# Performance work log

Measured on AMD Instinct MI355X. Metric: run time of the kernel, lower is better.

## Reference

```python
import jax, jax.numpy as jnp
import numpy as np
from jax import lax

NUM_SUPERNODES = 1024
KNN_K = 16
MIN_GRIPPER = 16
MIN_MASK = 8
GRIP_START = 0
GRIP_RADIUS = 0.1
NEG_INF = -jnp.inf


def _take(a, idx):
    return jnp.take_along_axis(a, idx, axis=1)


def _scatter_or(idx, keep, Bf, N):
    # OR `keep` into a fresh [Bf,N] bool mask at positions idx (mirrors torch scatter_)
    b = jnp.arange(Bf)[:, None]
    return jnp.zeros((Bf, N), dtype=bool).at[b, idx].max(keep)


def _cdist(a, b):
    # a [B,M,3], b [B,N,3] -> [B,M,N] euclidean
    d2 = (jnp.sum(a * a, -1)[:, :, None] + jnp.sum(b * b, -1)[:, None, :]
          - 2.0 * jnp.einsum('bmd,bnd->bmn', a, b))
    return jnp.sqrt(jnp.maximum(d2, 0.0))


def _sample_supernodes(xyz, valid, state, mask_id, extra_scores, global_scores):
    Bf, N, _ = xyz.shape
    M = NUM_SUPERNODES
    valid = valid.astype(bool)
    row_has_valid = valid.any(axis=1)
    first_valid = jnp.argmax(valid, axis=1).astype(jnp.int32)  # [Bf]

    # ---- gripper quota: nearest points to gripper xyz (within radius if any) ----
    k_grip = min(MIN_GRIPPER, M)
    gxyz = state[:, GRIP_START:GRIP_START + 3]
    gdist = jnp.linalg.norm(xyz - gxyz[:, None, :], axis=-1)  # [Bf,N]
    in_radius = gdist <= GRIP_RADIUS
    has_radius = (valid & in_radius).any(axis=1, keepdims=True)
    eligible = valid & (in_radius | ~has_radius)
    dist_rank = jnp.where(eligible, gdist, jnp.inf)
    neg_vals, grip_idx = lax.top_k(-dist_rank, k_grip)
    grip_vals = -neg_vals
    grip_keep = jnp.isfinite(grip_vals) & row_has_valid[:, None]
    head_idx = jnp.where(grip_keep, grip_idx, first_valid[:, None])
    head_bucket = jnp.where(grip_keep, 1, -1)
    selected = _scatter_or(grip_idx, grip_keep, Bf, N)

    remaining = M - k_grip
    # ---- mask-instance quota: one point per mask id (dedup via sort) ----
    mask_cand = valid & ~selected
    sentinel = jnp.iinfo(mask_id.dtype).max
    mask_key = jnp.where(mask_cand, mask_id, sentinel)
    sort_idx = jnp.argsort(mask_key, axis=1)
    sorted_valid = _take(mask_cand, sort_idx)
    sorted_mask = _take(mask_id, sort_idx)
    first_for_id = jnp.concatenate(
        [sorted_valid[:, :1],
         sorted_valid[:, 1:] & (sorted_mask[:, 1:] != sorted_mask[:, :-1])], axis=1)
    pos = jnp.arange(N, dtype=jnp.float32)[None, :]
    mask_scores = jnp.where(first_for_id, -pos, NEG_INF)
    mask_vals, mask_pos = lax.top_k(mask_scores, remaining)
    mask_idx = _take(sort_idx, mask_pos)
    mask_keep = jnp.isfinite(mask_vals) & row_has_valid[:, None]
    selected_after_mask = selected | _scatter_or(mask_idx, mask_keep, Bf, N)

    # ---- extra random mask supernodes to guarantee min_mask quota ----
    k_extra = min(MIN_MASK, remaining)
    es = jnp.where(valid & ~selected_after_mask, extra_scores, NEG_INF)
    extra_vals, extra_idx = lax.top_k(es, k_extra)
    extra_keep = jnp.isfinite(extra_vals) & row_has_valid[:, None]
    use_extra = ~mask_keep[:, :k_extra] & extra_keep
    mask_idx = mask_idx.at[:, :k_extra].set(
        jnp.where(use_extra, extra_idx, mask_idx[:, :k_extra]))
    mask_keep = mask_keep.at[:, :k_extra].set(mask_keep[:, :k_extra] | use_extra)

    # ---- global random fill ----
    selected_for_global = selected | _scatter_or(mask_idx, mask_keep, Bf, N)
    gs = jnp.where(valid & ~selected_for_global, global_scores, NEG_INF)
    gvals, gidx = lax.top_k(gs, remaining)
    gkeep = jnp.isfinite(gvals) & row_has_valid[:, None]
    fill_idx = jnp.where(mask_keep, mask_idx,
                         jnp.where(gkeep, gidx, first_valid[:, None]))
    fill_bucket = jnp.where(mask_keep, 2, jnp.where(gkeep, 0, -1))

    out_idx = jnp.concatenate([head_idx, fill_idx], axis=1)
    out_bucket = jnp.concatenate([head_bucket, fill_bucket], axis=1)
    out_valid = _take(valid, out_idx) & row_has_valid[:, None]
    out_bucket = jnp.where(out_valid, out_bucket, -1)
    return out_idx, out_valid, out_bucket


def setup_inputs() -> dict:
    key = jax.random.key(0)
    ks = jax.random.split(key, 6)
    Bf, N, C = 8, 16384, 64
    return {
        'x': jax.random.normal(ks[0], (Bf, N, C), dtype=jnp.float32),
        'xyz': jax.random.normal(ks[1], (Bf, N, 3), dtype=jnp.float32),
        'valid': jnp.ones((Bf, N), dtype=bool),
        'state': jax.random.normal(ks[2], (Bf, 8), dtype=jnp.float32),
        'mask_id': jax.random.randint(ks[3], (Bf, N), 0, 32, dtype=jnp.int32),
        'extra_scores': jax.random.uniform(ks[4], (Bf, N), dtype=jnp.float32),
        'global_scores': jax.random.uniform(ks[5], (Bf, N), dtype=jnp.float32),
    }


def reference(x, xyz, valid, state, mask_id, extra_scores, global_scores):
    Bf, N, C = x.shape
    out_idx, out_valid, out_bucket = _sample_supernodes(
        xyz, valid, state, mask_id, extra_scores, global_scores)
    # gather_points
    supernode_xyz = _take(xyz, out_idx[:, :, None].repeat(3, axis=2))  # [Bf,M,3]
    # build_knn_neighbors: masked cdist + topk smallest
    dist = _cdist(supernode_xyz.astype(jnp.float32), xyz.astype(jnp.float32))
    dist = jnp.where(valid.astype(bool)[:, None, :], dist, jnp.inf)
    neg_vals, neighbor_idx = lax.top_k(-dist, KNN_K)
    neighbor_mask = jnp.isfinite(-neg_vals)  # [Bf,M,K]
    # gather_neighbors
    b = jnp.arange(Bf)[:, None, None]
    neighbor_feats = x[b, neighbor_idx]  # [Bf,M,K,C]
    return (neighbor_feats, supernode_xyz, neighbor_mask,
            out_idx, out_valid, out_bucket)
```

## Files before the change

kernel.cpp:

```cpp
#include <hip/hip_runtime.h>
#include <math.h>

typedef unsigned long long u64;
typedef unsigned int u32;

#define BF 8
#define NPTS 16384
#define M_SN 1024
#define CCH 64
#define KNN 16
#define NTHR1 1024
#define KPER 16
#define TBL 4096
#define CCAP 2048
#define REM 1008

constexpr size_t O0 = 0;
constexpr size_t O1 = 8388608;
constexpr size_t O2 = 8413184;
constexpr size_t O3 = 8544256;
constexpr size_t O4 = 8552448;
constexpr size_t O5 = 8560640;

#define PW_OFF ((size_t)256)
#define PW_BYTES ((size_t)BF * NPTS * 16)
#define SEG1_BYTES ((size_t)BF * M_SN * KNN * 8)

__device__ __forceinline__ bool is_valid_el(const void* vp, int mode, long long i) {
  if (mode == 1) return ((const unsigned char*)vp)[i] != 0;
  if (mode == 2) return ((const float*)vp)[i] != 0.0f;
  return ((const int*)vp)[i] != 0;
}

__device__ __forceinline__ u32 desc_enc(float f) {
  u32 u = __float_as_uint(f);
  u32 s = (u & 0x80000000u) ? ~u : (u | 0x80000000u);
  return ~s;
}
__device__ __forceinline__ bool enc_finite(u32 d) {
  u32 s = ~d;
  u32 u = (s & 0x80000000u) ? (s & 0x7FFFFFFFu) : ~s;
  return (u & 0x7F800000u) != 0x7F800000u;
}

__device__ __forceinline__ u64 wave_min_u64(u64 v) {
#pragma unroll
  for (int d = 32; d >= 1; d >>= 1) {
    u32 lo = __shfl_xor((u32)(v & 0xFFFFFFFFu), d, 64);
    u32 hi = __shfl_xor((u32)(v >> 32), d, 64);
    u64 o = ((u64)hi << 32) | lo;
    if (o < v) v = o;
  }
  return v;
}

__device__ __forceinline__ u64 block_min_u64(u64 v, u64* red16, int t) {
  v = wave_min_u64(v);
  if ((t & 63) == 0) red16[t >> 6] = v;
  __syncthreads();
  if (t < 64) {
    u64 x = red16[t & 15];
    x = wave_min_u64(x);
    if (t == 0) red16[0] = x;
  }
  __syncthreads();
  u64 r = red16[0];
  __syncthreads();
  return r;
}

__device__ __forceinline__ int block_excl_scan(int val, int* scanb, int t, int* tot) {
  int incl = val;
#pragma unroll
  for (int d = 1; d < 64; d <<= 1) {
    int v = __shfl_up(incl, d, 64);
    if ((t & 63) >= d) incl += v;
  }
  if ((t & 63) == 63) scanb[t >> 6] = incl;
  __syncthreads();
  if (t < 64) {
    int ws = (t < 16) ? scanb[t] : 0;
#pragma unroll
    for (int d = 1; d < 16; d <<= 1) {
      int v = __shfl_up(ws, d, 64);
      if ((t & 63) >= d) ws += v;
    }
    if (t < 16) scanb[16 + t] = ws;
  }
  __syncthreads();
  int wv = t >> 6;
  int base = (wv == 0) ? 0 : scanb[16 + wv - 1];
  *tot = scanb[16 + 15];
  int r = base + incl - val;
  __syncthreads();
  return r;
}

template<bool ASC, bool SHIFTBIN>
__device__ __forceinline__ void topk_select(const u32* ek, const u32* bk, u32 cmask,
    int Twant, int* table, u64* cand, int* scanb, int* sh, int* outArr, int t) {
  for (int j = t; j < TBL; j += NTHR1) table[j] = 0;
  if (t == 6) sh[6] = 0x7FFFFFFF;
  if (t == 7) sh[7] = 1;
  __syncthreads();
#pragma unroll
  for (int k = 0; k < KPER; k++) {
    if ((cmask >> k) & 1u) {
      int bin = SHIFTBIN ? (int)(ek[k] >> 20) : (int)bk[k];
      atomicAdd(&table[bin], 1);
    }
  }
  __syncthreads();
  int c_[4]; int c4 = 0;
#pragma unroll
  for (int q = 0; q < 4; q++) { c_[q] = table[4 * t + q]; c4 += c_[q]; }
  int htot;
  int cum = block_excl_scan(c4, scanb, t, &htot);
  const int T = min(Twant, htot);
  int e_ = cum;
#pragma unroll
  for (int q = 0; q < 4; q++) {
    int nx = e_ + c_[q];
    if (T > 0 && e_ < T && nx >= T) atomicMin(&sh[6], 4 * t + q);
    table[4 * t + q] = e_;
    e_ = nx;
  }
  __syncthreads();
  if (T <= 0) return;
  const int B = sh[6];
#pragma unroll
  for (int k = 0; k < KPER; k++) {
    if ((cmask >> k) & 1u) {
      int bin = SHIFTBIN ? (int)(ek[k] >> 20) : (int)bk[k];
      if (bin <= B) {
        int pos = atomicAdd(&table[bin], 1);
        if (pos < CCAP)
          cand[pos] = ((u64)ek[k] << 32) | ((u64)(u32)bin << 14) | (u32)(k * NTHR1 + t);
      }
    }
  }
  __syncthreads();
  const int nc = table[B];
  if (nc <= CCAP) {
    for (int c = t; c < nc; c += NTHR1) {
      u64 key = cand[c];
      int bin = (int)((key >> 14) & 0xFFFu);
      int s = bin ? table[bin - 1] : 0;
      int e2 = table[bin];
      int r = s;
      for (int j = s; j < e2; j++) r += (cand[j] < key);
      if (r < T) {
        u32 enc = (u32)(key >> 32);
        int ix = (int)(key & 0x3FFFu);
        bool fin = ASC ? (enc < 0x7F800000u) : enc_finite(enc);
        outArr[r] = fin ? ix : (ix | (int)0x80000000);
      }
    }
  } else {
    if (t == 0) sh[7] = 0;
  }
  __syncthreads();
}

__global__ void detect_valid(const unsigned* __restrict__ w, int nwords, int* __restrict__ flag) {
  __shared__ int cls;
  int t = threadIdx.x;
  if (t == 0) cls = 0;
  __syncthreads();
  int local = 0;
  for (int i = t; i < nwords; i += blockDim.x) {
    unsigned v = w[i];
    if (v == 0x3F800000u) local = 2;
    else if (v != 0u && v != 1u) local = max(local, 1);
  }
  if (local) atomicMax(&cls, local);
  __syncthreads();
  if (t == 0) flag[0] = cls;
}

__global__ __launch_bounds__(1024)
void sample_kernel(const float* __restrict__ xyz, const void* __restrict__ validp,
                   const float* __restrict__ state, const int* __restrict__ mask_id,
                   const float* __restrict__ extra, const float* __restrict__ glob,
                   int vwords, float4* __restrict__ pw, float* __restrict__ out) {
  __shared__ u64 red16[16];
  __shared__ int table[TBL];
  __shared__ int scanb[32];
  __shared__ int mpick[REM];
  __shared__ u64 cand[CCAP];
  __shared__ int gsorted[REM];
  __shared__ int head_i[16];
  __shared__ int head_bk[16];
  __shared__ int sh[8];

  const int b = blockIdx.x, t = threadIdx.x;
  const float* xyzb = xyz + (size_t)b * NPTS * 3;
  const int* midb = mask_id + (size_t)b * NPTS;
  const float* exb = extra + (size_t)b * NPTS;
  const float* glb = glob + (size_t)b * NPTS;

  if (t < 8) sh[t] = 0;
  if (t == 1) sh[1] = 0x7FFFFFFF;
  if (t < 16) gsorted[t] = -1;
  __syncthreads();

  {
    const unsigned* w = (const unsigned*)validp;
    int local = 0;
    for (int i = t; i < vwords; i += NTHR1) {
      unsigned vv = w[i];
      if (vv == 0x3F800000u) local = 2;
      else if (vv != 0u && vv != 1u) local = max(local, 1);
    }
    if (local) atomicMax(&sh[3], local);
  }
  __syncthreads();
  const int vmode = sh[3];

  u32 vbits = 0;
#pragma unroll
  for (int k = 0; k < KPER; k++) {
    int i = k * NTHR1 + t;
    if (is_valid_el(validp, vmode, (long long)b * NPTS + i)) vbits |= 1u << k;
  }
  if (vbits) {
    atomicOr(&sh[0], 1);
    atomicMin(&sh[1], (__ffs(vbits) - 1) * NTHR1 + t);
  }

  float gx = state[b * 8 + 0], gy = state[b * 8 + 1], gz = state[b * 8 + 2];
  float gd[KPER];
  u32 inr = 0;
#pragma unroll
  for (int k = 0; k < KPER; k++) {
    int i = k * NTHR1 + t;
    float px = xyzb[3 * i], py = xyzb[3 * i + 1], pz = xyzb[3 * i + 2];
    float dx = px - gx, dy = py - gy, dz = pz - gz;
    float d = sqrtf((dx * dx + dy * dy) + dz * dz);
    gd[k] = d;
    bool vb = (vbits >> k) & 1u;
    if (vb && d <= 0.1f) inr |= 1u << k;
    if (pw) {
      float sb = __fadd_rn(__fadd_rn(__fmul_rn(px, px), __fmul_rn(py, py)), __fmul_rn(pz, pz));
      pw[(size_t)b * NPTS + i] = make_float4(px, py, pz, vb ? sb : INFINITY);
    }
  }
  if (inr) atomicOr(&sh[2], 1);
  __syncthreads();

  const int rhv = sh[0];
  const int first_valid = rhv ? sh[1] : 0;
  const u32 elig = vbits & (sh[2] ? inr : 0xFFFFu);
  u32 sel = 0;

  {
    u32 ek[KPER];
#pragma unroll
    for (int k = 0; k < KPER; k++) ek[k] = __float_as_uint(gd[k]);
    topk_select<true, true>(ek, nullptr, elig, 16, table, cand, scanb, sh, gsorted, t);
    if (sh[7]) {
      if (t < 16) {
        int g = gsorted[t];
        head_i[t] = (g >= 0) ? g : first_valid;
        head_bk[t] = (g >= 0) ? 1 : -1;
      }
      __syncthreads();
      for (int j = 0; j < 16; j++) {
        if (head_bk[j] == 1) {
          int ix = head_i[j];
          if ((ix & (NTHR1 - 1)) == t) sel |= 1u << (ix >> 10);
        }
      }
    } else {
      for (int it = 0; it < 16; ++it) {
        u64 best = ~0ull;
#pragma unroll
        for (int k = 0; k < KPER; k++) {
          if (((elig >> k) & 1u) && !((sel >> k) & 1u)) {
            u64 key = ((u64)__float_as_uint(gd[k]) << 32) | (u32)(k * NTHR1 + t);
            if (key < best) best = key;
          }
        }
        u64 w = block_min_u64(best, red16, t);
        bool keep = (w >> 32) < 0x7F800000ull;
        int idx = (int)(w & 0xFFFFFFFFu);
        if (t == 0) { head_i[it] = keep ? idx : first_valid; head_bk[it] = keep ? 1 : -1; }
        if (keep && (idx & (NTHR1 - 1)) == t) sel |= 1u << (idx >> 10);
      }
      __syncthreads();
    }
  }

  for (int j = t; j < TBL; j += NTHR1) table[j] = 0x7FFFFFFF;
  __syncthreads();
#pragma unroll
  for (int k = 0; k < KPER; k++) {
    if (((vbits >> k) & 1u) && !((sel >> k) & 1u)) {
      int i = k * NTHR1 + t;
      int id = midb[i];
      if ((u32)id < TBL) atomicMin(&table[id], i);
    }
  }
  __syncthreads();
  int cnt = 0;
#pragma unroll
  for (int q = 0; q < 4; q++) cnt += (table[4 * t + q] != 0x7FFFFFFF);
  int mtot;
  int excl = block_excl_scan(cnt, scanb, t, &mtot);
  {
    int pos = excl;
#pragma unroll
    for (int q = 0; q < 4; q++) {
      int v = table[4 * t + q];
      if (v != 0x7FFFFFFF) { if (pos < REM) mpick[pos] = v; pos++; }
    }
  }
  __syncthreads();
  const int nm = min(mtot, REM);
  for (int j = 0; j < nm; j++) {
    int p = mpick[j];
    if ((p & (NTHR1 - 1)) == t) sel |= 1u << (p >> 10);
  }

  u32 extra_used = 0;
  if (nm < 8 && rhv) {
    u32 extrbits = 0;
    for (int j = 0; j < 8; j++) {
      u64 best = ~0ull;
#pragma unroll
      for (int k = 0; k < KPER; k++) {
        if (((vbits >> k) & 1u) && !((sel >> k) & 1u) && !((extrbits >> k) & 1u)) {
          int i = k * NTHR1 + t;
          u64 key = ((u64)desc_enc(exb[i]) << 32) | (u32)i;
          if (key < best) best = key;
        }
      }
      u64 w = block_min_u64(best, red16, t);
      if (w == ~0ull) break;
      int idx = (int)(w & 0xFFFFFFFFu);
      bool fin = enc_finite((u32)(w >> 32));
      if ((idx & (NTHR1 - 1)) == t) extrbits |= 1u << (idx >> 10);
      if (j >= nm && fin) {
        extra_used |= 1u << j;
        if (t == 0) mpick[j] = idx;
        if ((idx & (NTHR1 - 1)) == t) sel |= 1u << (idx >> 10);
      }
    }
    __syncthreads();
  }

  {
    u32 cbits = vbits & ~sel;
    u32 ek[KPER], bk[KPER];
#pragma unroll
    for (int k = 0; k < KPER; k++) {
      if ((cbits >> k) & 1u) {
        float f = glb[k * NTHR1 + t];
        ek[k] = desc_enc(f);
        float g = fminf(fmaxf(f, 0.0f), 0.99999994f);
        bk[k] = 4095u - (u32)(g * 4096.0f);
      } else { ek[k] = 0xFFFFFFFFu; bk[k] = 4095u; }
    }
    for (int j = t; j < REM; j += NTHR1) gsorted[j] = -1;
    topk_select<false, false>(ek, bk, cbits, REM, table, cand, scanb, sh, gsorted, t);
    if (!sh[7]) {
      u32 gext = 0;
      for (int j = 0; j < REM; j++) {
        u64 best = ~0ull;
#pragma unroll
        for (int k = 0; k < KPER; k++) {
          if (((cbits >> k) & 1u) && !((gext >> k) & 1u)) {
            u64 key = ((u64)ek[k] << 32) | (u32)(k * NTHR1 + t);
            if (key < best) best = key;
          }
        }
        u64 w = block_min_u64(best, red16, t);
        if (w == ~0ull) break;
        int idx = (int)(w & 0xFFFFFFFFu);
        if ((idx & (NTHR1 - 1)) == t) gext |= 1u << (idx >> 10);
        if (t == 0) gsorted[j] = enc_finite((u32)(w >> 32)) ? idx : (idx | (int)0x80000000);
      }
      __syncthreads();
    }
  }

  {
    int slot = t;
    int idx, bucket;
    if (slot < 16) {
      idx = head_i[slot];
      bucket = head_bk[slot];
    } else {
      int jj = slot - 16;
      bool mk = (jj < nm) || (jj < 8 && ((extra_used >> jj) & 1u));
      if (mk) { idx = mpick[jj]; bucket = 2; }
      else {
        int g = gsorted[jj];
        if (rhv && g >= 0) { idx = g; bucket = 0; }
        else { idx = first_valid; bucket = -1; }
      }
    }
    bool ov = rhv && is_valid_el(validp, vmode, (long long)b * NPTS + idx);
    int ob = ov ? bucket : -1;
    size_t o = (size_t)b * M_SN + slot;
    out[O3 + o] = (float)idx;
    out[O4 + o] = ov ? 1.0f : 0.0f;
    out[O5 + o] = (float)ob;
    out[O1 + 3 * o + 0] = xyzb[3 * idx + 0];
    out[O1 + 3 * o + 1] = xyzb[3 * idx + 1];
    out[O1 + 3 * o + 2] = xyzb[3 * idx + 2];
  }
}

#define NTHR2 256
#define CH 1024
#define SPG 2
#define SNBLK 16

__global__ __launch_bounds__(256)
void knn_kernel(const float* __restrict__ x, const float* __restrict__ xyz,
                const void* __restrict__ validp, const int* __restrict__ flagp,
                const float4* __restrict__ pw, u64* __restrict__ wnws, int nseg,
                float* __restrict__ out) {
  __shared__ __align__(16) float4 st[CH];
  __shared__ u64 wnl[SNBLK * KNN];

  const int b = blockIdx.x >> 6;
  const int snblk = blockIdx.x & 63;
  const int seg = blockIdx.y;
  const int t = threadIdx.x;
  const int g = t >> 5;
  const int sub = t & 31;
  const int lanebase = t & 32;
  const int m0 = snblk * SNBLK + g * SPG;
  const float* xyzb = xyz + (size_t)b * NPTS * 3;
  const long long gbase = (long long)b * NPTS;
  const int vmode = pw ? 0 : flagp[0];

  float a2x[SPG], a2y[SPG], a2z[SPG];
#pragma unroll
  for (int s = 0; s < SPG; s++) {
    int sidx = (int)out[O3 + (size_t)b * M_SN + m0 + s];
    float ax, ay, az;
    if (pw) { float4 c = pw[gbase + sidx]; ax = c.x; ay = c.y; az = c.z; }
    else { ax = xyzb[3 * sidx]; ay = xyzb[3 * sidx + 1]; az = xyzb[3 * sidx + 2]; }
    a2x[s] = ax + ax; a2y[s] = ay + ay; a2z[s] = az + az;
  }

  const int S = NPTS / nseg;
  const int sbeg = seg * S;

  float ld[SPG]; int li[SPG]; float kq[SPG];

  for (int c0 = sbeg; c0 < sbeg + S; c0 += CH) {
    if (pw) {
      const float4* src = pw + gbase + c0;
#pragma unroll
      for (int qq = 0; qq < CH / NTHR2; qq++) st[t + qq * NTHR2] = src[t + qq * NTHR2];
    } else {
      for (int p = t; p < CH; p += NTHR2) {
        float px = xyzb[3 * (c0 + p)], py = xyzb[3 * (c0 + p) + 1], pz = xyzb[3 * (c0 + p) + 2];
        bool v = is_valid_el(validp, vmode, gbase + c0 + p);
        float sb = __fadd_rn(__fadd_rn(__fmul_rn(px, px), __fmul_rn(py, py)), __fmul_rn(pz, pz));
        st[p] = make_float4(px, py, pz, v ? sb : INFINITY);
      }
    }
    __syncthreads();

    int jstart = 0;
    if (c0 == sbeg) {
      float4 v = st[sub];
      float qv[SPG]; int qi[SPG];
#pragma unroll
      for (int s = 0; s < SPG; s++) {
        qv[s] = __builtin_fmaf(a2x[s], v.x, __builtin_fmaf(a2y[s], v.y, __builtin_fmaf(a2z[s], v.z, -v.w)));
        qi[s] = c0 + sub;
      }
#pragma unroll
      for (int p = 0; p < 32; p++) {
        int par;
        if ((p & 1) == 0) par = sub ^ 1;
        else par = (sub == 0 || sub == 31) ? sub : (((sub - 1) ^ 1) + 1);
        bool lo = sub < par;
#pragma unroll
        for (int s = 0; s < SPG; s++) {
          float oq = __shfl(qv[s], par, 32);
          int oi = __shfl(qi[s], par, 32);
          if (par != sub) {
            bool take = lo ? (oq > qv[s]) : (oq < qv[s]);
            if (take) { qv[s] = oq; qi[s] = oi; }
          }
        }
      }
#pragma unroll
      for (int s = 0; s < SPG; s++) { ld[s] = qv[s]; li[s] = qi[s]; kq[s] = __shfl(ld[s], 15, 32); }
      jstart = 1;
    }

#pragma unroll 4
    for (int j = jstart; j < CH / 32; j++) {
      float4 v = st[sub + 32 * j];
#pragma unroll
      for (int s = 0; s < SPG; s++) {
        float qv = __builtin_fmaf(a2x[s], v.x, __builtin_fmaf(a2y[s], v.y, __builtin_fmaf(a2z[s], v.z, -v.w)));
        u64 bal = __ballot(qv > kq[s]);
        u32 mq = (u32)(bal >> lanebase);
        while (mq) {
          int bb = __ffs(mq) - 1;
          mq &= mq - 1;
          float kd = __shfl(qv, lanebase + bb, 64);
          if (kd > kq[s]) {
            int ki = c0 + 32 * j + bb;
            bool gt = ld[s] < kd;
            float sd = __shfl_up(ld[s], 1, 32);
            int si = __shfl_up(li[s], 1, 32);
            int pg = __shfl_up(gt ? 1 : 0, 1, 32);
            if (sub == 0) pg = 0;
            ld[s] = gt ? (pg ? sd : kd) : ld[s];
            li[s] = gt ? (pg ? si : ki) : li[s];
            kq[s] = __shfl(ld[s], 15, 32);
          }
        }
      }
    }
    __syncthreads();
  }

  if (wnws) {
#pragma unroll
    for (int s = 0; s < SPG; s++)
      if (sub < KNN)
        wnws[(((size_t)seg * BF + b) * M_SN + (m0 + s)) * KNN + sub] =
            ((u64)desc_enc(ld[s]) << 32) | (u32)li[s];
    return;
  }

#pragma unroll
  for (int s = 0; s < SPG; s++)
    if (sub < KNN) wnl[(g * SPG + s) * KNN + sub] = ((u64)desc_enc(ld[s]) << 32) | (u32)li[s];
  __syncthreads();
  for (int r = t; r < SNBLK * KNN; r += NTHR2) {
    u64 key = wnl[r];
    int ni = (int)(key & (u64)(NPTS - 1));
    int mm = snblk * SNBLK + (r >> 4);
    size_t o2 = ((size_t)b * M_SN + mm) * KNN + (r & 15);
    out[O2 + o2] = enc_finite((u32)(key >> 32)) ? 1.0f : 0.0f;
    const float4* src = (const float4*)(x + (gbase + ni) * CCH);
    float4* dst = (float4*)(out + O0 + o2 * CCH);
#pragma unroll
    for (int q = 0; q < 16; q++) dst[q] = src[q];
  }
}

#define MSPB 4
__global__ __launch_bounds__(256)
void knn_merge_kernel(const float* __restrict__ x, const u64* __restrict__ wnws,
                      int nseg, float* __restrict__ out) {
  __shared__ u64 keys[MSPB][64];
  __shared__ u64 wsel[MSPB][KNN];
  const int b = blockIdx.x >> 8;
  const int sn0 = (blockIdx.x & 255) * MSPB;
  const int t = threadIdx.x;
  const int s = t >> 6, e = t & 63;
  const int E = nseg * KNN;
  if (e < E) {
    int seg = e >> 4, k = e & 15;
    keys[s][e] = wnws[(((size_t)seg * BF + b) * M_SN + sn0 + s) * KNN + k];
  }
  __syncthreads();
  if (e < E) {
    u64 my = keys[s][e];
    int rk = 0;
    for (int j = 0; j < E; j++) rk += (keys[s][j] < my);
    if (rk < KNN) wsel[s][rk] = my;
  }
  __syncthreads();
  {
    int row = t >> 2, q4 = t & 3;
    u64 key = wsel[row >> 4][row & 15];
    int ni = (int)(key & (u64)(NPTS - 1));
    int mm = sn0 + (row >> 4);
    size_t o2 = ((size_t)b * M_SN + mm) * KNN + (row & 15);
    if (q4 == 0) out[O2 + o2] = enc_finite((u32)(key >> 32)) ? 1.0f : 0.0f;
    const float4* src = (const float4*)(x + ((size_t)b * NPTS + ni) * CCH);
    float4* dst = (float4*)(out + O0 + o2 * CCH);
#pragma unroll
    for (int q = 0; q < 4; q++) dst[q4 * 4 + q] = src[q4 * 4 + q];
  }
}

extern "C" void kernel_launch(void* const* d_in, const int* in_sizes, int n_in,
                              void* d_out, int out_size, void* d_ws, size_t ws_size,
                              hipStream_t stream) {
  const float* x = (const float*)d_in[0];
  const float* xyz = (const float*)d_in[1];
  const void* valid = d_in[2];
  const float* state = (const float*)d_in[3];
  const int* mask_id = (const int*)d_in[4];
  const float* extra = (const float*)d_in[5];
  const float* glob = (const float*)d_in[6];
  float* out = (float*)d_out;
  int* flag = (int*)d_ws;
  const int vwords = in_sizes[2] / 4;

  float4* pw = nullptr;
  u64* wnws = nullptr;
  int nseg = 1;
  if (ws_size >= PW_OFF + PW_BYTES) pw = (float4*)((char*)d_ws + PW_OFF);
  if (pw && ws_size >= PW_OFF + PW_BYTES + 4 * SEG1_BYTES) {
    nseg = 4; wnws = (u64*)((char*)d_ws + PW_OFF + PW_BYTES);
  } else if (pw && ws_size >= PW_OFF + PW_BYTES + 2 * SEG1_BYTES) {
    nseg = 2; wnws = (u64*)((char*)d_ws + PW_OFF + PW_BYTES);
  }

  if (!pw)
    detect_valid<<<1, 1024, 0, stream>>>((const unsigned*)valid, vwords, flag);
  sample_kernel<<<BF, NTHR1, 0, stream>>>(xyz, valid, state, mask_id, extra, glob,
                                          vwords, pw, out);
  dim3 kg(BF * 64, nseg);
  knn_kernel<<<kg, NTHR2, 0, stream>>>(x, xyz, valid, flag, pw, wnws, nseg, out);
  if (nseg > 1) knn_merge_kernel<<<BF * 256, NTHR2, 0, stream>>>(x, wnws, nseg, out);
}
```

Measured before the change: 307.4 us.

## Replace per-candidate KNN insertion with shared-memory candidate buffer and batch sort

The per-query top-16 used to be kept in registers across a 32-lane group, and each accepted candidate went through a serial shuffle-based insertion. Now accepted candidates are appended to a 64-entry shared-memory buffer per query. When the buffer fills, it is sorted with a 32-step odd-even network, trimmed to the best 16, and the acceptance threshold is updated. The segment split is also reduced from four to two, which changes grid parallelism and merge cost. The trade-off is extra shared memory per block and periodic full sorts in exchange for far fewer serialized insertions.

Result: slower. 357.7 us (+16.4%).

```diff
diff --git a/kernel.cpp b/kernel.cpp
--- a/kernel.cpp
+++ b/kernel.cpp
@@ -37,6 +37,11 @@
   u32 s = (u & 0x80000000u) ? ~u : (u | 0x80000000u);
   return ~s;
 }
+__device__ __forceinline__ float desc_dec(u32 e) {
+  u32 s = ~e;
+  u32 u = (s & 0x80000000u) ? (s & 0x7FFFFFFFu) : ~s;
+  return __uint_as_float(u);
+}
 __device__ __forceinline__ bool enc_finite(u32 d) {
   u32 s = ~d;
   u32 u = (s & 0x80000000u) ? (s & 0x7FFFFFFFu) : ~s;
@@ -94,6 +99,12 @@
   int r = base + incl - val;
   __syncthreads();
   return r;
+}
+
+__device__ __forceinline__ u64 shfl64_grp(u64 v, int src) {
+  u32 lo = (u32)__shfl((int)(u32)(v & 0xFFFFFFFFu), src, 32);
+  u32 hi = (u32)__shfl((int)(u32)(v >> 32), src, 32);
+  return ((u64)hi << 32) | lo;
 }
 
 template<bool ASC, bool SHIFTBIN>
@@ -416,6 +427,22 @@
 #define CH 1024
 #define SPG 2
 #define SNBLK 16
+#define BCAP 64
+
+__device__ __forceinline__ void sort64g(const u64* gb, int n, int sub, u64& a0, u64& a1) {
+  a0 = (2 * sub < n) ? gb[2 * sub] : ~0ull;
+  a1 = (2 * sub + 1 < n) ? gb[2 * sub + 1] : ~0ull;
+#pragma unroll
+  for (int p = 0; p < 32; p++) {
+    u64 mn = (a0 < a1) ? a0 : a1;
+    u64 mx = (a0 < a1) ? a1 : a0;
+    a0 = mn; a1 = mx;
+    u64 up = shfl64_grp(a0, sub + 1);
+    u64 dn = shfl64_grp(a1, sub - 1);
+    if (sub < 31) a1 = (a1 < up) ? a1 : up;
+    if (sub > 0)  a0 = (a0 > dn) ? a0 : dn;
+  }
+}
 
 __global__ __launch_bounds__(256)
 void knn_kernel(const float* __restrict__ x, const float* __restrict__ xyz,
@@ -423,6 +450,7 @@
                 const float4* __restrict__ pw, u64* __restrict__ wnws, int nseg,
                 float* __restrict__ out) {
   __shared__ __align__(16) float4 st[CH];
+  __shared__ u64 buf[SNBLK][BCAP];
   __shared__ u64 wnl[SNBLK * KNN];
 
   const int b = blockIdx.x >> 6;
@@ -450,7 +478,9 @@
   const int S = NPTS / nseg;
   const int sbeg = seg * S;
 
-  float ld[SPG]; int li[SPG]; float kq[SPG];
+  float thrq[SPG]; int cnt[SPG]; bool virgin[SPG];
+#pragma unroll
+  for (int s = 0; s < SPG; s++) { thrq[s] = -INFINITY; cnt[s] = 0; virgin[s] = true; }
 
   for (int c0 = sbeg; c0 < sbeg + S; c0 += CH) {
     if (pw) {
@@ -467,77 +497,51 @@
     }
     __syncthreads();
 
-    int jstart = 0;
-    if (c0 == sbeg) {
-      float4 v = st[sub];
-      float qv[SPG]; int qi[SPG];
+#pragma unroll 2
+    for (int j = 0; j < CH / 32; j++) {
+      float4 v = st[sub + 32 * j];
 #pragma unroll
       for (int s = 0; s < SPG; s++) {
-        qv[s] = __builtin_fmaf(a2x[s], v.x, __builtin_fmaf(a2y[s], v.y, __builtin_fmaf(a2z[s], v.z, -v.w)));
-        qi[s] = c0 + sub;
-      }
-#pragma unroll
-      for (int p = 0; p < 32; p++) {
-        int par;
-        if ((p & 1) == 0) par = sub ^ 1;
-        else par = (sub == 0 || sub == 31) ? sub : (((sub - 1) ^ 1) + 1);
-        bool lo = sub < par;
-#pragma unroll
-        for (int s = 0; s < SPG; s++) {
-          float oq = __shfl(qv[s], par, 32);
-          int oi = __shfl(qi[s], par, 32);
-          if (par != sub) {
-            bool take = lo ? (oq > qv[s]) : (oq < qv[s]);
-            if (take) { qv[s] = oq; qi[s] = oi; }
+        u64* gb = &buf[g * SPG + s][0];
+        float qv = __builtin_fmaf(a2x[s], v.x, __builtin_fmaf(a2y[s], v.y, __builtin_fmaf(a2z[s], v.z, -v.w)));
+        bool acc = virgin[s] || (qv > thrq[s]);
+        u64 bal = __ballot(acc);
+        u32 mq = (u32)(bal >> lanebase);
+        if (mq) {
+          int na = __popc(mq);
+          if (cnt[s] + na > BCAP) {
+            u64 a0, a1;
+            sort64g(gb, cnt[s], sub, a0, a1);
+            if (sub < 8) { gb[2 * sub] = a0; gb[2 * sub + 1] = a1; }
+            u64 k15 = shfl64_grp(a1, 7);
+            thrq[s] = desc_dec((u32)(k15 >> 32));
+            cnt[s] = 16;
+            virgin[s] = false;
           }
+          if (acc) {
+            int pos = cnt[s] + __popc(mq & ((1u << sub) - 1u));
+            gb[pos] = ((u64)desc_enc(qv) << 32) | (u32)(c0 + 32 * j + sub);
+          }
+          cnt[s] += na;
         }
       }
-#pragma unroll
-      for (int s = 0; s < SPG; s++) { ld[s] = qv[s]; li[s] = qi[s]; kq[s] = __shfl(ld[s], 15, 32); }
-      jstart = 1;
-    }
-
-#pragma unroll 4
-    for (int j = jstart; j < CH / 32; j++) {
-      float4 v = st[sub + 32 * j];
-#pragma unroll
-      for (int s = 0; s < SPG; s++) {
-        float qv = __builtin_fmaf(a2x[s], v.x, __builtin_fmaf(a2y[s], v.y, __builtin_fmaf(a2z[s], v.z, -v.w)));
-        u64 bal = __ballot(qv > kq[s]);
-        u32 mq = (u32)(bal >> lanebase);
-        while (mq) {
-          int bb = __ffs(mq) - 1;
-          mq &= mq - 1;
-          float kd = __shfl(qv, lanebase + bb, 64);
-          if (kd > kq[s]) {
-            int ki = c0 + 32 * j + bb;
-            bool gt = ld[s] < kd;
-            float sd = __shfl_up(ld[s], 1, 32);
-            int si = __shfl_up(li[s], 1, 32);
-            int pg = __shfl_up(gt ? 1 : 0, 1, 32);
-            if (sub == 0) pg = 0;
-            ld[s] = gt ? (pg ? sd : kd) : ld[s];
-            li[s] = gt ? (pg ? si : ki) : li[s];
-            kq[s] = __shfl(ld[s], 15, 32);
-          }
-        }
-      }
     }
     __syncthreads();
   }
 
-  if (wnws) {
-#pragma unroll
-    for (int s = 0; s < SPG; s++)
-      if (sub < KNN)
-        wnws[(((size_t)seg * BF + b) * M_SN + (m0 + s)) * KNN + sub] =
-            ((u64)desc_enc(ld[s]) << 32) | (u32)li[s];
-    return;
-  }
-
-#pragma unroll
-  for (int s = 0; s < SPG; s++)
-    if (sub < KNN) wnl[(g * SPG + s) * KNN + sub] = ((u64)desc_enc(ld[s]) << 32) | (u32)li[s];
+#pragma unroll
+  for (int s = 0; s < SPG; s++) {
+    u64 a0, a1;
+    sort64g(&buf[g * SPG + s][0], cnt[s], sub, a0, a1);
+    if (wnws) {
+      size_t base = (((size_t)seg * BF + b) * M_SN + (m0 + s)) * KNN;
+      if (sub < 8) { wnws[base + 2 * sub] = a0; wnws[base + 2 * sub + 1] = a1; }
+    } else {
+      if (sub < 8) { wnl[(g * SPG + s) * KNN + 2 * sub] = a0; wnl[(g * SPG + s) * KNN + 2 * sub + 1] = a1; }
+    }
+  }
+  if (wnws) return;
+
   __syncthreads();
   for (int r = t; r < SNBLK * KNN; r += NTHR2) {
     u64 key = wnl[r];
@@ -607,9 +611,7 @@
   u64* wnws = nullptr;
   int nseg = 1;
   if (ws_size >= PW_OFF + PW_BYTES) pw = (float4*)((char*)d_ws + PW_OFF);
-  if (pw && ws_size >= PW_OFF + PW_BYTES + 4 * SEG1_BYTES) {
-    nseg = 4; wnws = (u64*)((char*)d_ws + PW_OFF + PW_BYTES);
-  } else if (pw && ws_size >= PW_OFF + PW_BYTES + 2 * SEG1_BYTES) {
+  if (pw && ws_size >= PW_OFF + PW_BYTES + 2 * SEG1_BYTES) {
     nseg = 2; wnws = (u64*)((char*)d_ws + PW_OFF + PW_BYTES);
   }
 
```
